# Performance work log

Hardware: AMD Instinct MI355X
Metric: run time of the kernel (lower is better)

Reference implementation:

```python
import jax, jax.numpy as jnp
import numpy as np

K_NN = 8        # neighbors
RADIUS = 0.1    # neighbor distance cutoff


def setup_inputs() -> dict:
    key = jax.random.key(0)
    k1, k2 = jax.random.split(key)
    B, N, KS = 2, 8192, 16  # batch, points, mask slots
    pc = jax.random.uniform(k1, (B, N, 3), dtype=jnp.float32)
    mask = jax.random.uniform(k2, (B, N, KS), dtype=jnp.float32)
    return {"pc": pc, "mask": mask}


def _knn(k, pc):
    # squared pairwise distances via gemm: (B,N,N)
    sq = jnp.sum(pc * pc, axis=-1)
    d2 = sq[:, :, None] + sq[:, None, :] - 2.0 * jnp.einsum("bnd,bmd->bnm", pc, pc)
    d2 = jnp.maximum(d2, 0.0)
    neg_d2, idx = jax.lax.top_k(-d2, k)          # k smallest distances
    dist = jnp.sqrt(jnp.maximum(-neg_d2, 0.0))   # (B,N,k) euclidean
    return dist, idx


def reference(pc, mask):
    # mask: (B,N,KS) -> (B,KS,N)
    mask_t = jnp.transpose(mask, (0, 2, 1))
    dist, idx = _knn(K_NN, pc)                   # (B,N,k) each
    # replace out-of-radius neighbors with the self index (nearest = self)
    self_idx = idx[:, :, :1]                     # (B,N,1)
    idx = jnp.where(dist > RADIUS, self_idx, idx)
    idx = jax.lax.stop_gradient(idx)
    # grouping_operation: (B,KS,N) gathered at (B,N,k) -> (B,KS,N,k)
    nn_mask = jax.vmap(lambda f, i: f[:, i])(mask_t, idx)
    # loss_norm=1: L1 norm over mask-slot dim (dim=1), mean over k, mean overall
    diff = mask_t[:, :, :, None] - nn_mask       # (B,KS,N,k)
    loss = jnp.sum(jnp.abs(diff), axis=1).mean(axis=-1)  # (B,N)
    return loss.mean()
```

## Files before the change

### kernel.cpp

```cpp
#include <hip/hip_runtime.h>

#define BATCH 2
#define NPTS  8192
#define KS    16
#define KNN   8
#define R2LOOSE 0.0101f
#define KEYMASK 0xFFFFE000u
#define NCELL   1000
#define CSTRIDE 1024

#define QB       64
#define NWAVE    8
#define NTHREADS 512
#define CAP      32
#define SLAB     256
#define NBLK     (BATCH * NPTS / QB)

__device__ __forceinline__ int cell_of(float x, float y, float z) {
    int cx = (int)(x * 10.0f); cx = cx > 9 ? 9 : cx;
    int cy = (int)(y * 10.0f); cy = cy > 9 ? 9 : cy;
    int cz = (int)(z * 10.0f); cz = cz > 9 ? 9 : cz;
    return (cx * 10 + cy) * 10 + cz;
}

__global__ __launch_bounds__(1024) void build_kernel(
    const float* __restrict__ pc,
    float4* __restrict__ cs, int* __restrict__ sidx,
    int* __restrict__ cstart, float* __restrict__ out)
{
    __shared__ int h[1024];
    __shared__ int wsum[16];
    const int blk = blockIdx.x, t = threadIdx.x;
    const int b = blk >> 3, seg = blk & 7;
    const int lane = t & 63, w = t >> 6;

    h[t] = 0;
    if (blk == 0 && t == 0) out[0] = 0.0f;

    const float* p = pc + (size_t)b * NPTS * 3;
    float X[8], Y[8], Z[8]; int CC[8];
#pragma unroll
    for (int j = 0; j < 8; ++j) {
        const int i = j * 1024 + t;
        X[j] = p[3 * i]; Y[j] = p[3 * i + 1]; Z[j] = p[3 * i + 2];
        CC[j] = cell_of(X[j], Y[j], Z[j]);
    }
    __syncthreads();

    int myold = 0;
#pragma unroll
    for (int j = 0; j < 8; ++j) {
        const int old = atomicAdd(&h[CC[j]], 1);
        if (j == seg) myold = old;
        __syncthreads();
    }

    const int sum = h[t];
    int inc = sum;
#pragma unroll
    for (int off = 1; off < 64; off <<= 1) {
        const int v = __shfl_up(inc, off);
        if (lane >= off) inc += v;
    }
    if (lane == 63) wsum[w] = inc;
    __syncthreads();
    if (w == 0) {
        const int v = (lane < 16) ? wsum[lane] : 0;
        int iv = v;
#pragma unroll
        for (int off = 1; off < 16; off <<= 1) {
            const int u = __shfl_up(iv, off);
            if (lane >= off) iv += u;
        }
        if (lane < 16) wsum[lane] = iv - v;
    }
    __syncthreads();
    const int excl = inc - sum + wsum[w];
    if (seg == 0) cstart[b * CSTRIDE + t] = excl;
    __syncthreads();
    h[t] = excl;
    __syncthreads();

    float mx = X[0], my_ = Y[0], mz = Z[0]; int mc = CC[0];
#pragma unroll
    for (int j = 1; j < 8; ++j)
        if (seg == j) { mx = X[j]; my_ = Y[j]; mz = Z[j]; mc = CC[j]; }

    const int pos = h[mc] + myold;
    const float sq = fmaf(mz, mz, fmaf(my_, my_, mx * mx));
    cs[b * NPTS + pos]   = make_float4(mx, my_, mz, -0.5f * sq);
    sidx[b * NPTS + pos] = seg * 1024 + t;
}

#define CEX(a, b) { const unsigned mn_ = min(a, b), mx_ = max(a, b); \
                    a = mn_; b = mx_; }

__global__ __launch_bounds__(512) void knn_loss_kernel(
    const float4* __restrict__ cs,
    const int*    __restrict__ sidx,
    const int*    __restrict__ cstart,
    const float*  __restrict__ mask,
    float* __restrict__ out)
{
    __shared__ float4   stg4[NWAVE][SLAB];
    __shared__ int      stgi[NWAVE][SLAB];
    __shared__ unsigned sbuf[CAP * NTHREADS];
    __shared__ int      fidx[QB * KNN];
    __shared__ int      qid[QB];
    __shared__ float    red[NWAVE];

    const int t = threadIdx.x;
    const int l = t & 63;
    const int k = l & 7;
    const int s = t >> 6;
    const int su = __builtin_amdgcn_readfirstlane(s);
    const int Q = (t >> 3) & 63;
    const int blk = blockIdx.x;
    const int b  = blk >> 7;
    const int q0 = (blk & 127) * QB;
    const int qpos = q0 + Q;

    const float4* csb = cs + b * NPTS;
    const float4 qc = csb[qpos];
    const int    qi = sidx[b * NPTS + qpos];
    if (k == 0) qid[Q] = qi;

    const float qx = qc.x, qy = qc.y, qz = qc.z;
    const float qs = -2.0f * qc.w;
    const float negthr = (qs - R2LOOSE) * 0.5f;
    const unsigned SENT = (__float_as_uint(R2LOOSE) & KEYMASK) | 0x1FFFu;

    int lex = cell_of(qx, qy, qz);
    int cmn = lex, cmx = lex;
#pragma unroll
    for (int off = 32; off; off >>= 1) {
        cmn = min(cmn, __shfl_xor(cmn, off));
        cmx = max(cmx, __shfl_xor(cmx, off));
    }
    const int cfirst = __builtin_amdgcn_readfirstlane(cmn);
    const int clast  = __builtin_amdgcn_readfirstlane(cmx);

    const int* csp = cstart + b * CSTRIDE;
    int P[9], L[9], cum[9];
    int run = 0, Cw = 0;
    const int offs[9] = {-110, -100, -90, -10, 0, 10, 90, 100, 110};
#pragma unroll
    for (int i = 0; i < 9; ++i) {
        int lo = cfirst + offs[i] - 1;
        int hp = clast + offs[i] + 2;
        lo = min(max(lo, 0), 1000);
        hp = min(max(hp, 0), 1000);
        lo = max(lo, run);
        hp = max(hp, lo);
        run = hp;
        const int p = csp[lo], e = csp[hp];
        P[i] = p; cum[i] = Cw; L[i] = e - p; Cw += L[i];
    }

    int cnt = 0;
    auto EVAL = [&](const float4& c, int spos) {
        const float tt = fmaf(c.x, qx, fmaf(c.y, qy, fmaf(c.z, qz, c.w)));
        const float d2 = fmaxf(fmaf(-2.0f, tt, qs), 0.0f);
        const unsigned key =
            (__float_as_uint(d2) & KEYMASK) | (unsigned)spos;
        const int slot = cnt < (CAP - 1) ? cnt : (CAP - 1);
        sbuf[slot * NTHREADS + t] = key;
        cnt += (tt >= negthr) ? 1 : 0;
    };

    for (int fb = 0; fb < Cw; fb += SLAB) {
        const int n = min(SLAB, Cw - fb);
        for (int f = l; f < n; f += 64) {
            const int g = fb + f;
            int sp = P[0] + g;
#pragma unroll
            for (int i = 1; i < 9; ++i)
                sp = (g >= cum[i]) ? P[i] + (g - cum[i]) : sp;
            stg4[su][f] = csb[sp];
            stgi[su][f] = sp;
        }
        asm volatile("s_waitcnt lgkmcnt(0)" ::: "memory");

        for (int j = k; j < n; j += 8) {
            const float4 c = stg4[su][j];
            const int   sp = stgi[su][j];
            EVAL(c, sp);
        }
        asm volatile("s_waitcnt lgkmcnt(0)" ::: "memory");
    }

    unsigned md[KNN];
#pragma unroll
    for (int kk = 0; kk < KNN; ++kk) md[kk] = SENT;
    const int m = cnt < CAP ? cnt : CAP;
    for (int kk = 0; kk < m; ++kk) {
        unsigned ky = sbuf[kk * NTHREADS + t];
#pragma unroll
        for (int i = 0; i < KNN; ++i) {
            const unsigned mn = min(ky, md[i]);
            const unsigned mx = max(ky, md[i]);
            md[i] = mn; ky = mx;
        }
    }

#pragma unroll
    for (int off = 1; off <= 4; off <<= 1) {
        unsigned bb[8], cc[8];
#pragma unroll
        for (int j = 0; j < 8; ++j)
            bb[j] = (unsigned)__shfl_xor((int)md[j], off);
#pragma unroll
        for (int j = 0; j < 8; ++j)
            cc[j] = min(md[j], bb[7 - j]);
        CEX(cc[0], cc[4]); CEX(cc[1], cc[5]);
        CEX(cc[2], cc[6]); CEX(cc[3], cc[7]);
        CEX(cc[0], cc[2]); CEX(cc[1], cc[3]);
        CEX(cc[4], cc[6]); CEX(cc[5], cc[7]);
        CEX(cc[0], cc[1]); CEX(cc[2], cc[3]);
        CEX(cc[4], cc[5]); CEX(cc[6], cc[7]);
#pragma unroll
        for (int j = 0; j < 8; ++j) md[j] = cc[j];
    }

    {
        const unsigned ky = md[k];
        int nb;
        if (ky >= SENT) {
            nb = qi;
        } else {
            const int sp = (int)(ky & 0x1FFFu);
            const float4 cc2 = csb[sp];
            const float dx = cc2.x - qx;
            const float dy = cc2.y - qy;
            const float dz = cc2.z - qz;
            const float d2 = fmaf(dx, dx, fmaf(dy, dy, dz * dz));
            nb = (sqrtf(d2) > 0.1f) ? qi : sidx[b * NPTS + sp];
        }
        fidx[Q * KNN + k] = nb;
    }
    __syncthreads();

    const int q2 = t >> 3;
    const int j2 = t & 7;
    const int qg = qid[q2];
    const int nb = fidx[q2 * KNN + j2];
    const float* mrow = mask + ((size_t)b * NPTS + qg) * KS;
    const float* nrow = mask + ((size_t)b * NPTS + nb) * KS;
    float acc = 0.0f;
#pragma unroll
    for (int c = 0; c < KS; c += 4) {
        const float4 a = *(const float4*)(mrow + c);
        const float4 v = *(const float4*)(nrow + c);
        acc += fabsf(a.x - v.x) + fabsf(a.y - v.y) +
               fabsf(a.z - v.z) + fabsf(a.w - v.w);
    }

#pragma unroll
    for (int off = 32; off > 0; off >>= 1) acc += __shfl_down(acc, off);
    if ((t & 63) == 0) red[s] = acc;
    __syncthreads();
    if (t == 0) {
        float sum = 0.0f;
#pragma unroll
        for (int i = 0; i < NWAVE; ++i) sum += red[i];
        atomicAdd(out, sum * (1.0f / (BATCH * NPTS * KNN)));
    }
}

extern "C" void kernel_launch(void* const* d_in, const int* in_sizes, int n_in,
                              void* d_out, int out_size, void* d_ws, size_t ws_size,
                              hipStream_t stream) {
    const float* pc   = (const float*)d_in[0];
    const float* mask = (const float*)d_in[1];
    float* out = (float*)d_out;

    float4* cs     = (float4*)d_ws;
    int*    sidx   = (int*)((char*)d_ws + 262144);
    int*    cstart = (int*)((char*)d_ws + 327680);

    hipLaunchKernelGGL(build_kernel, dim3(16), dim3(1024), 0, stream,
                       pc, cs, sidx, cstart, out);
    hipLaunchKernelGGL(knn_loss_kernel, dim3(NBLK), dim3(512), 0, stream,
                       cs, sidx, cstart, mask, out);
}
```

Measured before the change: 71.82 us.

## Use register top-8 insertion with 16 lanes per query, dropping LDS candidate buffer

Each query is now handled by 16 lanes instead of 8, with 32 queries per block, so twice as many blocks are launched. The 64KB shared candidate buffer is removed: each lane inserts every candidate straight into a register-resident sorted top-8 through a compare-exchange chain. Out-of-radius candidates become max-key sentinels. This frees LDS and raises occupancy (launch bounds 512,4). The trade-off is eight compare-exchanges per candidate instead of one conditional store, plus an extra shuffle-merge stage across 16 lanes. The final loss gather is split so each lane handles half of the 16 mask slots.

```diff
diff --git a/kernel.cpp b/kernel.cpp
--- a/kernel.cpp
+++ b/kernel.cpp
@@ -9,10 +9,9 @@
 #define NCELL   1000
 #define CSTRIDE 1024
 
-#define QB       64
+#define QB       32
 #define NWAVE    8
 #define NTHREADS 512
-#define CAP      32
 #define SLAB     256
 #define NBLK     (BATCH * NPTS / QB)
 
@@ -95,29 +94,28 @@
 #define CEX(a, b) { const unsigned mn_ = min(a, b), mx_ = max(a, b); \
                     a = mn_; b = mx_; }
 
-__global__ __launch_bounds__(512) void knn_loss_kernel(
+__global__ __launch_bounds__(512, 4) void knn_loss_kernel(
     const float4* __restrict__ cs,
     const int*    __restrict__ sidx,
     const int*    __restrict__ cstart,
     const float*  __restrict__ mask,
     float* __restrict__ out)
 {
-    __shared__ float4   stg4[NWAVE][SLAB];
-    __shared__ int      stgi[NWAVE][SLAB];
-    __shared__ unsigned sbuf[CAP * NTHREADS];
-    __shared__ int      fidx[QB * KNN];
-    __shared__ int      qid[QB];
-    __shared__ float    red[NWAVE];
+    __shared__ float4 stg4[NWAVE][SLAB];
+    __shared__ int    stgi[NWAVE][SLAB];
+    __shared__ int    fidx[QB * KNN];
+    __shared__ int    qid[QB];
+    __shared__ float  red[NWAVE];
 
     const int t = threadIdx.x;
     const int l = t & 63;
-    const int k = l & 7;
+    const int k = l & 15;
     const int s = t >> 6;
     const int su = __builtin_amdgcn_readfirstlane(s);
-    const int Q = (t >> 3) & 63;
+    const int Q = t >> 4;
     const int blk = blockIdx.x;
-    const int b  = blk >> 7;
-    const int q0 = (blk & 127) * QB;
+    const int b  = blk >> 8;
+    const int q0 = (blk & 255) * QB;
     const int qpos = q0 + Q;
 
     const float4* csb = cs + b * NPTS;
@@ -141,7 +139,7 @@
     const int clast  = __builtin_amdgcn_readfirstlane(cmx);
 
     const int* csp = cstart + b * CSTRIDE;
-    int P[9], L[9], cum[9];
+    int P[9], cum[9];
     int run = 0, Cw = 0;
     const int offs[9] = {-110, -100, -90, -10, 0, 10, 90, 100, 110};
 #pragma unroll
@@ -154,18 +152,20 @@
         hp = max(hp, lo);
         run = hp;
         const int p = csp[lo], e = csp[hp];
-        P[i] = p; cum[i] = Cw; L[i] = e - p; Cw += L[i];
-    }
-
-    int cnt = 0;
+        P[i] = p; cum[i] = Cw; Cw += e - p;
+    }
+
+    unsigned md[KNN];
+#pragma unroll
+    for (int kk = 0; kk < KNN; ++kk) md[kk] = SENT;
     auto EVAL = [&](const float4& c, int spos) {
         const float tt = fmaf(c.x, qx, fmaf(c.y, qy, fmaf(c.z, qz, c.w)));
         const float d2 = fmaxf(fmaf(-2.0f, tt, qs), 0.0f);
-        const unsigned key =
-            (__float_as_uint(d2) & KEYMASK) | (unsigned)spos;
-        const int slot = cnt < (CAP - 1) ? cnt : (CAP - 1);
-        sbuf[slot * NTHREADS + t] = key;
-        cnt += (tt >= negthr) ? 1 : 0;
+        unsigned ky = (tt >= negthr)
+            ? ((__float_as_uint(d2) & KEYMASK) | (unsigned)spos)
+            : 0xFFFFFFFFu;
+#pragma unroll
+        for (int i = 0; i < KNN; ++i) CEX(md[i], ky);
     };
 
     for (int fb = 0; fb < Cw; fb += SLAB) {
@@ -181,30 +181,20 @@
         }
         asm volatile("s_waitcnt lgkmcnt(0)" ::: "memory");
 
-        for (int j = k; j < n; j += 8) {
-            const float4 c = stg4[su][j];
-            const int   sp = stgi[su][j];
-            EVAL(c, sp);
-        }
+        int j = k;
+        for (; j + 16 < n; j += 32) {
+            const float4 c0 = stg4[su][j];
+            const float4 c1 = stg4[su][j + 16];
+            const int   s0 = stgi[su][j];
+            const int   s1 = stgi[su][j + 16];
+            EVAL(c0, s0); EVAL(c1, s1);
+        }
+        if (j < n) { const float4 c0 = stg4[su][j]; EVAL(c0, stgi[su][j]); }
         asm volatile("s_waitcnt lgkmcnt(0)" ::: "memory");
     }
 
-    unsigned md[KNN];
-#pragma unroll
-    for (int kk = 0; kk < KNN; ++kk) md[kk] = SENT;
-    const int m = cnt < CAP ? cnt : CAP;
-    for (int kk = 0; kk < m; ++kk) {
-        unsigned ky = sbuf[kk * NTHREADS + t];
-#pragma unroll
-        for (int i = 0; i < KNN; ++i) {
-            const unsigned mn = min(ky, md[i]);
-            const unsigned mx = max(ky, md[i]);
-            md[i] = mn; ky = mx;
-        }
-    }
-
-#pragma unroll
-    for (int off = 1; off <= 4; off <<= 1) {
+#pragma unroll
+    for (int off = 1; off <= 8; off <<= 1) {
         unsigned bb[8], cc[8];
 #pragma unroll
         for (int j = 0; j < 8; ++j)
@@ -222,7 +212,7 @@
         for (int j = 0; j < 8; ++j) md[j] = cc[j];
     }
 
-    {
+    if (k < KNN) {
         const unsigned ky = md[k];
         int nb;
         if (ky >= SENT) {
@@ -240,15 +230,16 @@
     }
     __syncthreads();
 
-    const int q2 = t >> 3;
-    const int j2 = t & 7;
+    const int q2 = t >> 4;
+    const int j2 = (t >> 1) & 7;
+    const int hf = t & 1;
     const int qg = qid[q2];
     const int nb = fidx[q2 * KNN + j2];
-    const float* mrow = mask + ((size_t)b * NPTS + qg) * KS;
-    const float* nrow = mask + ((size_t)b * NPTS + nb) * KS;
+    const float* mrow = mask + ((size_t)b * NPTS + qg) * KS + hf * 8;
+    const float* nrow = mask + ((size_t)b * NPTS + nb) * KS + hf * 8;
     float acc = 0.0f;
 #pragma unroll
-    for (int c = 0; c < KS; c += 4) {
+    for (int c = 0; c < 8; c += 4) {
         const float4 a = *(const float4*)(mrow + c);
         const float4 v = *(const float4*)(nrow + c);
         acc += fabsf(a.x - v.x) + fabsf(a.y - v.y) +
@@ -280,6 +271,6 @@
 
     hipLaunchKernelGGL(build_kernel, dim3(16), dim3(1024), 0, stream,
                        pc, cs, sidx, cstart, out);
-    hipLaunchKernelGGL(knn_loss_kernel, dim3(NBLK), dim3(512), 0, stream,
+    hipLaunchKernelGGL(knn_loss_kernel, dim3(NBLK), dim3(NTHREADS), 0, stream,
                        cs, sidx, cstart, mask, out);
 }
```

After: 72.61 us. No clear change (+1.1%).
